# Kernel tuning notes

Hardware: AMD Instinct MI355X
Metric: run time of the kernel (lower is better)

Reference implementation:

```python
import jax, jax.numpy as jnp
import numpy as np

N_HEADS, D_MODEL, D_HEAD = 16, 1024, 64
INIT_RANGE = 0.02
IGNORE = -100000.0


def setup_inputs() -> dict:
    key = jax.random.key(0)
    ks = jax.random.split(key, 5)
    x = jax.random.normal(ks[0], (2, 2048, D_MODEL), dtype=jnp.float32)
    Qs = jax.random.normal(ks[1], (N_HEADS, D_MODEL, D_HEAD), dtype=jnp.float32) * INIT_RANGE
    Ks = jax.random.normal(ks[2], (N_HEADS, D_MODEL, D_HEAD), dtype=jnp.float32) * INIT_RANGE
    Vs = jax.random.normal(ks[3], (N_HEADS, D_MODEL, D_HEAD), dtype=jnp.float32) * INIT_RANGE
    O = jax.random.normal(ks[4], (N_HEADS, D_HEAD, D_MODEL), dtype=jnp.float32) * INIT_RANGE
    Qbs = jnp.zeros((N_HEADS, D_HEAD), dtype=jnp.float32)
    Kbs = jnp.zeros((N_HEADS, D_HEAD), dtype=jnp.float32)
    Vbs = jnp.zeros((N_HEADS, D_HEAD), dtype=jnp.float32)
    Ob = jnp.zeros((D_MODEL,), dtype=jnp.float32)
    return {"normalized_resid_pre": x, "Qs": Qs, "Qbs": Qbs, "Ks": Ks, "Kbs": Kbs,
            "Vs": Vs, "Vbs": Vbs, "O": O, "Ob": Ob}


def reference(normalized_resid_pre, Qs, Qbs, Ks, Kbs, Vs, Vbs, O, Ob):
    x = normalized_resid_pre  # [b, p, d]
    q = jnp.einsum('bpd,hdk->bphk', x, Qs) + Qbs  # [b, p, h, k]
    k = jnp.einsum('bpd,hdk->bphk', x, Ks) + Kbs
    v = jnp.einsum('bpd,hdk->bphk', x, Vs) + Vbs
    scores = jnp.einsum('bqhk,bshk->bhqs', q, k) / np.sqrt(D_HEAD)  # [b, h, Q, K]
    S = scores.shape[-1]
    causal = jnp.triu(jnp.ones((S, S), dtype=bool), k=1)
    scores = jnp.where(causal, jnp.float32(IGNORE), scores)
    pattern = jax.nn.softmax(scores, axis=-1)
    z = jnp.einsum('bshk,bhqs->bqhk', v, pattern)
    attn_out = jnp.einsum('bqhk,hkd->bqd', z, O) + Ob
    return attn_out
```

## Files before the change

### kernel.cpp

```cpp
#include <hip/hip_runtime.h>

#define BB 2
#define SS 2048
#define DM 1024
#define NH 16
#define DH 64
#define BP (BB*SS)
#define BHSD (BB*NH*SS*DH)

typedef __attribute__((ext_vector_type(8))) short short8v;
typedef __attribute__((ext_vector_type(4))) float float4v;

__device__ __forceinline__ unsigned short f2bf(float f) {
    unsigned int u = __float_as_uint(f);
    u += 0x7fffu + ((u >> 16) & 1u);
    return (unsigned short)(u >> 16);
}

__device__ __forceinline__ void async_cp16(const void* g, void* l) {
    __builtin_amdgcn_global_load_lds(
        (const __attribute__((address_space(1))) unsigned int*)g,
        (__attribute__((address_space(3))) unsigned int*)l, 16, 0, 0);
}

__global__ __launch_bounds__(256) void k_cvtx(const float* __restrict__ x,
                                              unsigned short* __restrict__ xb) {
    const size_t i = (size_t)blockIdx.x * 256 + threadIdx.x;
    const float4 a = ((const float4*)x)[i * 2];
    const float4 b = ((const float4*)x)[i * 2 + 1];
    uint4 o;
    o.x = f2bf(a.x) | ((unsigned)f2bf(a.y) << 16);
    o.y = f2bf(a.z) | ((unsigned)f2bf(a.w) << 16);
    o.z = f2bf(b.x) | ((unsigned)f2bf(b.y) << 16);
    o.w = f2bf(b.z) | ((unsigned)f2bf(b.w) << 16);
    ((uint4*)xb)[i] = o;
}

__global__ __launch_bounds__(256) void k_wrepack(
    const float* __restrict__ Qs, const float* __restrict__ Ks,
    const float* __restrict__ Vs, const float* __restrict__ O,
    unsigned short* __restrict__ WbT, unsigned short* __restrict__ ObT)
{
    __shared__ float t[64][65];
    const int z = blockIdx.z;
    const float* src; unsigned short* dst; int C;
    if (z < 48) {
        if (blockIdx.y != 0) return;
        const int set = z >> 4, h = z & 15;
        src = ((set == 0) ? Qs : (set == 1) ? Ks : Vs) + (size_t)h * DM * DH;
        dst = WbT + (size_t)z * DH * DM;
        C = DH;
    } else { src = O; dst = ObT; C = DM; }
    const int r0 = blockIdx.x * 64, c0 = blockIdx.y * 64;
    const int tid = threadIdx.x, c = tid & 63, r4 = tid >> 6;
    #pragma unroll
    for (int i = 0; i < 16; ++i) {
        int r = r4 + i * 4;
        t[r][c] = src[(size_t)(r0 + r) * C + c0 + c];
    }
    __syncthreads();
    #pragma unroll
    for (int i = 0; i < 16; ++i) {
        int rr = r4 + i * 4;
        dst[(size_t)(c0 + rr) * DM + r0 + c] = f2bf(t[c][rr]);
    }
}

__global__ __launch_bounds__(256) void k_vt(const unsigned short* __restrict__ v,
                                            unsigned short* __restrict__ vT) {
    __shared__ unsigned short t[64][66];
    const int bh = blockIdx.y;
    const int s0 = blockIdx.x * 64;
    const unsigned short* src = v + (size_t)bh * SS * DH + (size_t)s0 * DH;
    unsigned short* dst = vT + (size_t)bh * DH * SS + s0;
    const int tid = threadIdx.x, c = tid & 63, r4 = tid >> 6;
    #pragma unroll
    for (int i = 0; i < 16; ++i) { int r = r4 + i * 4; t[r][c] = src[r * DH + c]; }
    __syncthreads();
    #pragma unroll
    for (int i = 0; i < 16; ++i) { int dr = r4 + i * 4; dst[(size_t)dr * SS + c] = t[c][dr]; }
}

template<int MODE>
__global__ __launch_bounds__(256) void k_gemm(
    const unsigned short* __restrict__ A, const unsigned short* __restrict__ Bm,
    void* __restrict__ Cout, int N, int K,
    const float* __restrict__ bq, const float* __restrict__ bk,
    const float* __restrict__ bv)
{
    __shared__ __align__(16) unsigned short Al[128 * 32];
    __shared__ __align__(16) unsigned short Bl[128 * 32];
    const int tid = threadIdx.x;
    const int w = tid >> 6, l = tid & 63;
    const int ll = l & 15, lh = l >> 4;
    const int m0 = blockIdx.x * 128, n0 = blockIdx.y * 128;
    const int wm = w >> 1, wn = w & 1;
    const int sr = l >> 2, sc = l & 3;

    const float4v vzero = {0.f, 0.f, 0.f, 0.f};
    float4v acc[4][4];
    #pragma unroll
    for (int i = 0; i < 4; ++i)
        #pragma unroll
        for (int j = 0; j < 4; ++j) acc[i][j] = vzero;

    for (int k0 = 0; k0 < K; k0 += 32) {
        __syncthreads();
        #pragma unroll
        for (int half = 0; half < 2; ++half) {
            const int r = w * 32 + half * 16 + sr;
            async_cp16(A + (size_t)(m0 + r) * K + k0 + sc * 8,
                       &Al[(w * 32 + half * 16) * 32]);
            async_cp16(Bm + (size_t)(n0 + r) * K + k0 + sc * 8,
                       &Bl[(w * 32 + half * 16) * 32]);
        }
        __syncthreads();

        short8v af[4], bfr[4];
        #pragma unroll
        for (int mi = 0; mi < 4; ++mi)
            af[mi] = *(const short8v*)&Al[(wm * 64 + mi * 16 + ll) * 32 + lh * 8];
        #pragma unroll
        for (int ni = 0; ni < 4; ++ni)
            bfr[ni] = *(const short8v*)&Bl[(wn * 64 + ni * 16 + ll) * 32 + lh * 8];
        #pragma unroll
        for (int mi = 0; mi < 4; ++mi)
            #pragma unroll
            for (int ni = 0; ni < 4; ++ni)
                acc[mi][ni] = __builtin_amdgcn_mfma_f32_16x16x32_bf16(
                    af[mi], bfr[ni], acc[mi][ni], 0, 0, 0);
    }

    #pragma unroll
    for (int mi = 0; mi < 4; ++mi)
        #pragma unroll
        for (int ni = 0; ni < 4; ++ni)
            #pragma unroll
            for (int r = 0; r < 4; ++r) {
                const int gm = m0 + wm * 64 + mi * 16 + lh * 4 + r;
                const int gn = n0 + wn * 64 + ni * 16 + ll;
                float val = acc[mi][ni][r];
                if (MODE == 0) {
                    const int set = gn >> 10, h = (gn >> 6) & 15, dh = gn & 63;
                    const float* bias = (set == 0) ? bq : (set == 1) ? bk : bv;
                    val += bias[(h << 6) + dh];
                    const int b_ = gm >> 11, s = gm & 2047;
                    ((unsigned short*)Cout)[(size_t)set * BHSD +
                        (((size_t)(b_ * NH + h) * SS + s) << 6) + dh] = f2bf(val);
                } else {
                    val += bq[gn];
                    ((float*)Cout)[(size_t)gm * N + gn] = val;
                }
            }
}

__global__ __launch_bounds__(256) void k_attn(
    const unsigned short* __restrict__ qg, const unsigned short* __restrict__ kg,
    const unsigned short* __restrict__ vtg, unsigned short* __restrict__ zg)
{
    __shared__ __align__(16) float Plds[4][16][68];
    const int tid = threadIdx.x, w = tid >> 6, l = tid & 63;
    const int ll = l & 15, lh = l >> 4;
    const int qt = (int)gridDim.x - 1 - (int)blockIdx.x;
    const int bh = blockIdx.y;
    const int q0 = qt * 64 + w * 16;
    const unsigned short* qb = qg + (size_t)bh * SS * DH;
    const unsigned short* kb = kg + (size_t)bh * SS * DH;
    const unsigned short* vb = vtg + (size_t)bh * DH * SS;

    short8v qf[2];
    qf[0] = *(const short8v*)(qb + (size_t)(q0 + ll) * DH + lh * 8);
    qf[1] = *(const short8v*)(qb + (size_t)(q0 + ll) * DH + 32 + lh * 8);

    const float4v vzero = {0.f, 0.f, 0.f, 0.f};
    float4v zacc[4];
    #pragma unroll
    for (int n = 0; n < 4; ++n) zacc[n] = vzero;
    float mrow[4] = {-1e30f, -1e30f, -1e30f, -1e30f};
    float lrow[4] = {0.f, 0.f, 0.f, 0.f};

    for (int jt = 0; jt <= qt; ++jt) {
        const unsigned short* kt = kb + (size_t)jt * 64 * DH;
        float4v sv[4];
        #pragma unroll
        for (int n = 0; n < 4; ++n) {
            short8v kf0 = *(const short8v*)(kt + (size_t)(n * 16 + ll) * DH + lh * 8);
            short8v kf1 = *(const short8v*)(kt + (size_t)(n * 16 + ll) * DH + 32 + lh * 8);
            float4v t = vzero;
            t = __builtin_amdgcn_mfma_f32_16x16x32_bf16(qf[0], kf0, t, 0, 0, 0);
            t = __builtin_amdgcn_mfma_f32_16x16x32_bf16(qf[1], kf1, t, 0, 0, 0);
            sv[n] = t;
        }
        const bool diag = (jt == qt);
        #pragma unroll
        for (int n = 0; n < 4; ++n)
            #pragma unroll
            for (int r = 0; r < 4; ++r) {
                float xv = sv[n][r] * 0.125f;
                if (diag && (jt * 64 + n * 16 + ll) > (q0 + lh * 4 + r)) xv = -1e30f;
                sv[n][r] = xv;
            }
        #pragma unroll
        for (int r = 0; r < 4; ++r) {
            float mx = fmaxf(fmaxf(sv[0][r], sv[1][r]), fmaxf(sv[2][r], sv[3][r]));
            #pragma unroll
            for (int o = 1; o < 16; o <<= 1) mx = fmaxf(mx, __shfl_xor(mx, o, 64));
            const float mn = fmaxf(mrow[r], mx);
            const float corr = __expf(mrow[r] - mn);
            mrow[r] = mn;
            float rs = 0.f;
            #pragma unroll
            for (int n = 0; n < 4; ++n) {
                const float p = __expf(sv[n][r] - mn);
                sv[n][r] = p; rs += p;
            }
            #pragma unroll
            for (int o = 1; o < 16; o <<= 1) rs += __shfl_xor(rs, o, 64);
            lrow[r] = lrow[r] * corr + rs;
            #pragma unroll
            for (int n = 0; n < 4; ++n) zacc[n][r] *= corr;
            #pragma unroll
            for (int n = 0; n < 4; ++n) Plds[w][lh * 4 + r][n * 16 + ll] = sv[n][r];
        }
        short8v pa[2];
        #pragma unroll
        for (int kk = 0; kk < 2; ++kk)
            #pragma unroll
            for (int j = 0; j < 8; ++j)
                pa[kk][j] = (short)f2bf(Plds[w][ll][kk * 32 + lh * 8 + j]);
        const unsigned short* vt = vb + jt * 64;
        #pragma unroll
        for (int n = 0; n < 4; ++n) {
            short8v vf0 = *(const short8v*)(vt + (size_t)(n * 16 + ll) * SS + lh * 8);
            short8v vf1 = *(const short8v*)(vt + (size_t)(n * 16 + ll) * SS + 32 + lh * 8);
            zacc[n] = __builtin_amdgcn_mfma_f32_16x16x32_bf16(pa[0], vf0, zacc[n], 0, 0, 0);
            zacc[n] = __builtin_amdgcn_mfma_f32_16x16x32_bf16(pa[1], vf1, zacc[n], 0, 0, 0);
        }
    }

    const int b_ = bh >> 4, h = bh & 15;
    float inv[4];
    #pragma unroll
    for (int r = 0; r < 4; ++r) inv[r] = 1.f / lrow[r];
    #pragma unroll
    for (int n = 0; n < 4; ++n)
        #pragma unroll
        for (int r = 0; r < 4; ++r) {
            const int s = qt * 64 + w * 16 + lh * 4 + r;
            zg[(((size_t)(b_ * SS + s)) << 10) + (h << 6) + n * 16 + ll] =
                f2bf(zacc[n][r] * inv[r]);
        }
}

extern "C" void kernel_launch(void* const* d_in, const int* in_sizes, int n_in,
                              void* d_out, int out_size, void* d_ws, size_t ws_size,
                              hipStream_t stream)
{
    const float* x   = (const float*)d_in[0];
    const float* Qs  = (const float*)d_in[1];
    const float* Qbs = (const float*)d_in[2];
    const float* Ks  = (const float*)d_in[3];
    const float* Kbs = (const float*)d_in[4];
    const float* Vs  = (const float*)d_in[5];
    const float* Vbs = (const float*)d_in[6];
    const float* O   = (const float*)d_in[7];
    const float* Ob  = (const float*)d_in[8];

    unsigned short* xb  = (unsigned short*)d_ws;
    unsigned short* WbT = xb  + (size_t)BP * DM;
    unsigned short* ObT = WbT + (size_t)3 * NH * DH * DM;
    unsigned short* qkv = ObT + (size_t)DM * DM;
    unsigned short* vT  = qkv + (size_t)3 * BHSD;
    unsigned short* z   = vT  + (size_t)BHSD;

    k_cvtx<<<dim3(BP * DM / 2048), 256, 0, stream>>>(x, xb);
    k_wrepack<<<dim3(16, 16, 49), 256, 0, stream>>>(Qs, Ks, Vs, O, WbT, ObT);
    k_gemm<0><<<dim3(BP / 128, 3 * DM / 128), 256, 0, stream>>>(
        xb, WbT, qkv, 3 * DM, DM, Qbs, Kbs, Vbs);
    k_vt<<<dim3(SS / 64, BB * NH), 256, 0, stream>>>(qkv + (size_t)2 * BHSD, vT);
    k_attn<<<dim3(SS / 64, BB * NH), 256, 0, stream>>>(qkv, qkv + BHSD, vT, z);
    k_gemm<1><<<dim3(BP / 128, DM / 128), 256, 0, stream>>>(
        z, ObT, d_out, DM, DM, Ob, nullptr, nullptr);
}
```

Baseline: 382.0 us.

## Prefetch K/V fragments in attention, remap grid per XCD, defer row-sum reduction

The attention kernel now prefetches the next K tile and the current V tile into registers at the start of each iteration, so global loads overlap the MFMA and softmax work. It flattens the grid into one dimension and remaps block IDs so each XCD handles a contiguous group of batch-heads, which is meant to improve L2 reuse of K/V. The per-iteration cross-lane row-sum shuffle is deferred to one reduction at the end, and setprio hints wrap the MFMA sections. A launch-bounds occupancy hint of 3 blocks per CU is added, which raises register pressure risk given the extra prefetch registers.

```diff
diff --git a/kernel.cpp b/kernel.cpp
--- a/kernel.cpp
+++ b/kernel.cpp
@@ -15,6 +15,10 @@
     unsigned int u = __float_as_uint(f);
     u += 0x7fffu + ((u >> 16) & 1u);
     return (unsigned short)(u >> 16);
+}
+
+__device__ __forceinline__ short8v ld8(const unsigned short* p) {
+    return *(const short8v*)p;
 }
 
 __device__ __forceinline__ void async_cp16(const void* g, void* l) {
@@ -154,23 +158,25 @@
             }
 }
 
-__global__ __launch_bounds__(256) void k_attn(
+__global__ __launch_bounds__(256, 3) void k_attn(
     const unsigned short* __restrict__ qg, const unsigned short* __restrict__ kg,
     const unsigned short* __restrict__ vtg, unsigned short* __restrict__ zg)
 {
     __shared__ __align__(16) float Plds[4][16][68];
     const int tid = threadIdx.x, w = tid >> 6, l = tid & 63;
     const int ll = l & 15, lh = l >> 4;
-    const int qt = (int)gridDim.x - 1 - (int)blockIdx.x;
-    const int bh = blockIdx.y;
+    const unsigned bid = blockIdx.x;
+    const unsigned xcd = bid & 7, within = bid >> 3;
+    const int bh = (int)((xcd << 2) | (within >> 5));
+    const int qt = 31 - (int)(within & 31);
     const int q0 = qt * 64 + w * 16;
     const unsigned short* qb = qg + (size_t)bh * SS * DH;
     const unsigned short* kb = kg + (size_t)bh * SS * DH;
     const unsigned short* vb = vtg + (size_t)bh * DH * SS;
 
     short8v qf[2];
-    qf[0] = *(const short8v*)(qb + (size_t)(q0 + ll) * DH + lh * 8);
-    qf[1] = *(const short8v*)(qb + (size_t)(q0 + ll) * DH + 32 + lh * 8);
+    qf[0] = ld8(qb + (size_t)(q0 + ll) * DH + lh * 8);
+    qf[1] = ld8(qb + (size_t)(q0 + ll) * DH + 32 + lh * 8);
 
     const float4v vzero = {0.f, 0.f, 0.f, 0.f};
     float4v zacc[4];
@@ -179,18 +185,41 @@
     float mrow[4] = {-1e30f, -1e30f, -1e30f, -1e30f};
     float lrow[4] = {0.f, 0.f, 0.f, 0.f};
 
+    short8v kf[8];
+    #pragma unroll
+    for (int n = 0; n < 4; ++n) {
+        kf[n * 2]     = ld8(kb + (size_t)(n * 16 + ll) * DH + lh * 8);
+        kf[n * 2 + 1] = ld8(kb + (size_t)(n * 16 + ll) * DH + 32 + lh * 8);
+    }
+
     for (int jt = 0; jt <= qt; ++jt) {
-        const unsigned short* kt = kb + (size_t)jt * 64 * DH;
+        const unsigned short* vt = vb + jt * 64;
+        short8v vf[8];
+        #pragma unroll
+        for (int n = 0; n < 4; ++n) {
+            vf[n * 2]     = ld8(vt + (size_t)(n * 16 + ll) * SS + lh * 8);
+            vf[n * 2 + 1] = ld8(vt + (size_t)(n * 16 + ll) * SS + 32 + lh * 8);
+        }
+        const int jn = (jt < qt) ? jt + 1 : jt;
+        const unsigned short* ktn = kb + (size_t)jn * 64 * DH;
+        short8v nkf[8];
+        #pragma unroll
+        for (int n = 0; n < 4; ++n) {
+            nkf[n * 2]     = ld8(ktn + (size_t)(n * 16 + ll) * DH + lh * 8);
+            nkf[n * 2 + 1] = ld8(ktn + (size_t)(n * 16 + ll) * DH + 32 + lh * 8);
+        }
+
         float4v sv[4];
+        __builtin_amdgcn_s_setprio(1);
         #pragma unroll
         for (int n = 0; n < 4; ++n) {
-            short8v kf0 = *(const short8v*)(kt + (size_t)(n * 16 + ll) * DH + lh * 8);
-            short8v kf1 = *(const short8v*)(kt + (size_t)(n * 16 + ll) * DH + 32 + lh * 8);
             float4v t = vzero;
-            t = __builtin_amdgcn_mfma_f32_16x16x32_bf16(qf[0], kf0, t, 0, 0, 0);
-            t = __builtin_amdgcn_mfma_f32_16x16x32_bf16(qf[1], kf1, t, 0, 0, 0);
+            t = __builtin_amdgcn_mfma_f32_16x16x32_bf16(qf[0], kf[n * 2], t, 0, 0, 0);
+            t = __builtin_amdgcn_mfma_f32_16x16x32_bf16(qf[1], kf[n * 2 + 1], t, 0, 0, 0);
             sv[n] = t;
         }
+        __builtin_amdgcn_s_setprio(0);
+
         const bool diag = (jt == qt);
         #pragma unroll
         for (int n = 0; n < 4; ++n)
@@ -200,6 +229,7 @@
                 if (diag && (jt * 64 + n * 16 + ll) > (q0 + lh * 4 + r)) xv = -1e30f;
                 sv[n][r] = xv;
             }
+
         #pragma unroll
         for (int r = 0; r < 4; ++r) {
             float mx = fmaxf(fmaxf(sv[0][r], sv[1][r]), fmaxf(sv[2][r], sv[3][r]));
@@ -208,40 +238,47 @@
             const float mn = fmaxf(mrow[r], mx);
             const float corr = __expf(mrow[r] - mn);
             mrow[r] = mn;
-            float rs = 0.f;
+            float ps = 0.f;
             #pragma unroll
             for (int n = 0; n < 4; ++n) {
                 const float p = __expf(sv[n][r] - mn);
-                sv[n][r] = p; rs += p;
+                sv[n][r] = p; ps += p;
             }
-            #pragma unroll
-            for (int o = 1; o < 16; o <<= 1) rs += __shfl_xor(rs, o, 64);
-            lrow[r] = lrow[r] * corr + rs;
+            lrow[r] = lrow[r] * corr + ps;
             #pragma unroll
             for (int n = 0; n < 4; ++n) zacc[n][r] *= corr;
             #pragma unroll
             for (int n = 0; n < 4; ++n) Plds[w][lh * 4 + r][n * 16 + ll] = sv[n][r];
         }
+
         short8v pa[2];
         #pragma unroll
         for (int kk = 0; kk < 2; ++kk)
             #pragma unroll
             for (int j = 0; j < 8; ++j)
                 pa[kk][j] = (short)f2bf(Plds[w][ll][kk * 32 + lh * 8 + j]);
-        const unsigned short* vt = vb + jt * 64;
+
+        __builtin_amdgcn_s_setprio(1);
         #pragma unroll
         for (int n = 0; n < 4; ++n) {
-            short8v vf0 = *(const short8v*)(vt + (size_t)(n * 16 + ll) * SS + lh * 8);
-            short8v vf1 = *(const short8v*)(vt + (size_t)(n * 16 + ll) * SS + 32 + lh * 8);
-            zacc[n] = __builtin_amdgcn_mfma_f32_16x16x32_bf16(pa[0], vf0, zacc[n], 0, 0, 0);
-            zacc[n] = __builtin_amdgcn_mfma_f32_16x16x32_bf16(pa[1], vf1, zacc[n], 0, 0, 0);
-        }
-    }
-
+            zacc[n] = __builtin_amdgcn_mfma_f32_16x16x32_bf16(pa[0], vf[n * 2], zacc[n], 0, 0, 0);
+            zacc[n] = __builtin_amdgcn_mfma_f32_16x16x32_bf16(pa[1], vf[n * 2 + 1], zacc[n], 0, 0, 0);
+        }
+        __builtin_amdgcn_s_setprio(0);
+
+        #pragma unroll
+        for (int t = 0; t < 8; ++t) kf[t] = nkf[t];
+    }
+
+    float inv[4];
+    #pragma unroll
+    for (int r = 0; r < 4; ++r) {
+        float s = lrow[r];
+        #pragma unroll
+        for (int o = 1; o < 16; o <<= 1) s += __shfl_xor(s, o, 64);
+        inv[r] = 1.f / s;
+    }
     const int b_ = bh >> 4, h = bh & 15;
-    float inv[4];
-    #pragma unroll
-    for (int r = 0; r < 4; ++r) inv[r] = 1.f / lrow[r];
     #pragma unroll
     for (int n = 0; n < 4; ++n)
         #pragma unroll
@@ -278,7 +315,7 @@
     k_gemm<0><<<dim3(BP / 128, 3 * DM / 128), 256, 0, stream>>>(
         xb, WbT, qkv, 3 * DM, DM, Qbs, Kbs, Vbs);
     k_vt<<<dim3(SS / 64, BB * NH), 256, 0, stream>>>(qkv + (size_t)2 * BHSD, vT);
-    k_attn<<<dim3(SS / 64, BB * NH), 256, 0, stream>>>(qkv, qkv + BHSD, vT, z);
+    k_attn<<<dim3(SS / 64 * BB * NH), 256, 0, stream>>>(qkv, qkv + BHSD, vT, z);
     k_gemm<1><<<dim3(BP / 128, DM / 128), 256, 0, stream>>>(
         z, ObT, d_out, DM, DM, Ob, nullptr, nullptr);
 }
```

New measurement: 332.3 us. 13.0% less time.
